# Kernel optimization log

Hardware: AMD Instinct MI355X
Metric: run time of the kernel (lower is better)

The kernel has to match this reference:

```python
import jax, jax.numpy as jnp
import numpy as np
from jax import lax

B, L, H, K = 64, 1024, 768, 4
C1, C2 = 0.1, 0.1


def crf_marginals(feats, maskf, T):
    """Batched linear-chain CRF forward-backward.
    feats: [B,L,K] emission scores, maskf: [B,L] float (1=valid), T: [K,K] transitions.
    Returns marginals [B,L,K] (zeroed at padded positions)."""
    a0 = feats[:, 0]  # [B,K]

    def fwd_step(a, xs):
        f_t, m_t = xs  # [B,K], [B]
        new = f_t + jax.nn.logsumexp(a[:, :, None] + T[None], axis=1)
        a = jnp.where(m_t[:, None] > 0, new, a)  # freeze alpha past last valid token
        return a, a

    _, alphas_rest = lax.scan(fwd_step, a0,
                              (jnp.swapaxes(feats[:, 1:], 0, 1), maskf[:, 1:].T))
    alphas = jnp.concatenate([a0[None], alphas_rest], axis=0)  # [L,B,K]
    logZ = jax.nn.logsumexp(alphas[-1], axis=-1)  # [B] (alpha frozen at last valid t)

    bL = jnp.zeros_like(a0)

    def bwd_step(b, xs):
        f_n, m_n = xs  # emission/mask at t+1
        new = jax.nn.logsumexp(T[None] + (f_n + b)[:, None, :], axis=2)
        b = jnp.where(m_n[:, None] > 0, new, b)  # beta stays 0 until last valid token
        return b, b

    xs = (jnp.swapaxes(feats[:, 1:][:, ::-1], 0, 1), maskf[:, 1:][:, ::-1].T)
    _, betas_rev = lax.scan(bwd_step, bL, xs)
    betas = jnp.concatenate([bL[None], betas_rev], axis=0)[::-1]  # [L,B,K]

    marg = jnp.exp(alphas + betas - logZ[None, :, None]) * maskf.T[:, :, None]
    return jnp.swapaxes(marg, 0, 1)  # [B,L,K]


def _forward(hidden, maskf, w, b, T):
    feats = hidden @ w.T + b                      # [B,L,K] feat2tri
    marg = crf_marginals(feats, maskf, T)
    sp = marg[:, :, 1]                            # select_polarities, masked [B,L]
    gamma = sp.sum(axis=1) / 2.0                  # [B]
    sent_vs = jnp.einsum('bl,blh->bh', sp, hidden) / gamma[:, None]
    s_prob = sp / gamma[:, None]                  # padded-ragged per-token probs
    s_prob_norm = jnp.abs(s_prob).sum(axis=1).mean()
    pena = jax.nn.relu(T[1, 0] - T[0, 0]) + jax.nn.relu(T[0, 1] - T[1, 1])
    norm_pen = C1 * pena + C2 * s_prob_norm
    return sent_vs, norm_pen, s_prob


def setup_inputs():
    key = jax.random.key(0)
    ks = jax.random.split(key, 8)
    hidden = jax.random.normal(ks[0], (B, L, H), dtype=jnp.float32)
    seq_lens = jax.random.randint(ks[1], (B,), L // 4, L + 1)
    # hidden_mask: 0 for valid tokens, nonzero for padding (forward uses mask = hidden_mask==0)
    hidden_mask = (jnp.arange(L)[None, :] >= seq_lens[:, None]).astype(jnp.int32)
    subj_position = jax.random.randint(ks[2], (B, L), -20, 21)
    obj_position = jax.random.randint(ks[3], (B, L), -20, 21)
    pe_inputs = jax.random.randint(ks[4], (B, L), 0, 2 * L)
    pe_binary = jax.random.randint(ks[5], (B, L), 0, 2)
    w_feat2tri = jax.random.normal(ks[6], (K, H), dtype=jnp.float32) * (1.0 / np.sqrt(H)).astype(np.float32)
    b_feat2tri = jnp.zeros((K,), dtype=jnp.float32)
    transitions = jax.random.normal(ks[7], (K, K), dtype=jnp.float32) * 0.1
    return dict(hidden=hidden, hidden_mask=hidden_mask, subj_position=subj_position,
                obj_position=obj_position, seq_lens=seq_lens, pe_inputs=pe_inputs,
                pe_binary=pe_binary, w_feat2tri=w_feat2tri, b_feat2tri=b_feat2tri,
                transitions=transitions)


def reference(hidden, hidden_mask, subj_position, obj_position, seq_lens, pe_inputs,
              pe_binary, w_feat2tri, b_feat2tri, transitions):
    maskf = (hidden_mask == 0).astype(hidden.dtype)
    # relevance is computed in the original forward but never consumed downstream,
    # so it has no effect on outputs; omitted here.
    return _forward(hidden, maskf, w_feat2tri, b_feat2tri, transitions)
```

## Files before the change

### kernel.cpp

```cpp
#include <hip/hip_runtime.h>

#define B 64
#define L 1024
#define H 768
#define NROWS (B * L)
#define LOG2E 1.4426950408889634f
#define CS 16
#define NCH 64
#define NG 16

#define EXP2(x) __builtin_amdgcn_exp2f(x)
#define LOG2(x) __builtin_amdgcn_logf(x)

__device__ __forceinline__ void renorm4(float& x0, float& x1, float& x2, float& x3, float& lc) {
    const float g = fmaxf(fmaxf(x0, x1), fmaxf(x2, x3));
    const int e = (__float_as_int(g) >> 23) & 255;
    const float s = __int_as_float((254 - e) << 23);
    x0 *= s; x1 *= s; x2 *= s; x3 *= s;
    lc += (float)(e - 127);
}

__global__ __launch_bounds__(256) void feats_kernel(
    const float* __restrict__ hidden, const float* __restrict__ w,
    const float* __restrict__ bias, float4* __restrict__ pfeatsT)
{
    const int lane = threadIdx.x & 63;
    const int wave = (blockIdx.x * blockDim.x + threadIdx.x) >> 6;
    const int nwaves = (gridDim.x * blockDim.x) >> 6;

    float wr[3][4][4];
#pragma unroll
    for (int c = 0; c < 3; ++c)
#pragma unroll
        for (int j = 0; j < 4; ++j)
#pragma unroll
            for (int k = 0; k < 4; ++k)
                wr[c][j][k] = w[k * H + lane * 4 + 256 * c + j];
    const float bb0 = bias[0], bb1 = bias[1], bb2 = bias[2], bb3 = bias[3];

    for (int row = wave; row < NROWS; row += nwaves) {
        const float4* hrow = reinterpret_cast<const float4*>(hidden) + (size_t)row * (H / 4);
        float acc[4] = {0.f, 0.f, 0.f, 0.f};
#pragma unroll
        for (int c = 0; c < 3; ++c) {
            float4 h = hrow[lane + 64 * c];
            const float hv[4] = {h.x, h.y, h.z, h.w};
#pragma unroll
            for (int j = 0; j < 4; ++j)
#pragma unroll
                for (int k = 0; k < 4; ++k)
                    acc[k] = fmaf(hv[j], wr[c][j][k], acc[k]);
        }
#pragma unroll
        for (int k = 0; k < 4; ++k) {
            float v = acc[k];
#pragma unroll
            for (int s = 32; s >= 1; s >>= 1) v += __shfl_xor(v, s, 64);
            acc[k] = v;
        }
        if (lane == 0) {
            const int b = row >> 10, l = row & 1023;
            pfeatsT[l * B + b] = make_float4(EXP2((acc[0] + bb0) * LOG2E),
                                             EXP2((acc[1] + bb1) * LOG2E),
                                             EXP2((acc[2] + bb2) * LOG2E),
                                             EXP2((acc[3] + bb3) * LOG2E));
        }
    }
}

__global__ __launch_bounds__(128) void chunkmat_kernel(
    const float4* __restrict__ pfeatsT, const int* __restrict__ seq_lens,
    const float* __restrict__ T, float* __restrict__ mats_p,
    float* __restrict__ mats_lc)
{
    const int b = threadIdx.x & 63;
    const int dir = threadIdx.x >> 6;
    const int c = blockIdx.x;
    const int sl = seq_lens[b];
    const int lo = c * CS + 1;
    const int hi = min(c * CS + CS, L - 1);
    const int ns = hi - lo + 1;

    float eT2[4][4];
#pragma unroll
    for (int i = 0; i < 4; ++i)
#pragma unroll
        for (int j = 0; j < 4; ++j) eT2[i][j] = EXP2(T[i * 4 + j] * LOG2E);

    float4 fr[CS];
#pragma unroll
    for (int u = 0; u < CS; ++u) {
        const int t = dir ? max(hi - u, lo) : min(lo + u, hi);
        fr[u] = pfeatsT[t * B + b];
    }

    float M[4][4];
#pragma unroll
    for (int i = 0; i < 4; ++i)
#pragma unroll
        for (int j = 0; j < 4; ++j) M[i][j] = (i == j) ? 1.f : 0.f;
    float lc = 0.f;

#pragma unroll
    for (int u = 0; u < CS; ++u) {
        const int pos = dir ? (hi - u) : (lo + u);
        const bool valid = (u < ns) && (pos < sl);
        const float f[4] = {fr[u].x, fr[u].y, fr[u].z, fr[u].w};
        float nM[4][4];
        if (dir == 0) {
#pragma unroll
            for (int i = 0; i < 4; ++i)
#pragma unroll
                for (int j = 0; j < 4; ++j) {
                    const float s = (M[i][0] * eT2[0][j] + M[i][1] * eT2[1][j]) +
                                    (M[i][2] * eT2[2][j] + M[i][3] * eT2[3][j]);
                    nM[i][j] = s * f[j];
                }
        } else {
            float Mg[4][4];
#pragma unroll
            for (int k = 0; k < 4; ++k)
#pragma unroll
                for (int j = 0; j < 4; ++j) Mg[k][j] = f[k] * M[k][j];
#pragma unroll
            for (int i = 0; i < 4; ++i)
#pragma unroll
                for (int j = 0; j < 4; ++j)
                    nM[i][j] = (eT2[i][0] * Mg[0][j] + eT2[i][1] * Mg[1][j]) +
                               (eT2[i][2] * Mg[2][j] + eT2[i][3] * Mg[3][j]);
        }
#pragma unroll
        for (int i = 0; i < 4; ++i)
#pragma unroll
            for (int j = 0; j < 4; ++j) M[i][j] = valid ? nM[i][j] : M[i][j];

        if (u == 7 || u == CS - 1) {
            float g = 0.f;
#pragma unroll
            for (int i = 0; i < 4; ++i)
#pragma unroll
                for (int j = 0; j < 4; ++j) g = fmaxf(g, M[i][j]);
            const int e = (__float_as_int(g) >> 23) & 255;
            const float s = __int_as_float((254 - e) << 23);
#pragma unroll
            for (int i = 0; i < 4; ++i)
#pragma unroll
                for (int j = 0; j < 4; ++j) M[i][j] *= s;
            lc += (float)(e - 127);
        }
    }
#pragma unroll
    for (int i = 0; i < 4; ++i)
#pragma unroll
        for (int j = 0; j < 4; ++j)
            mats_p[((dir * NCH + c) * 16 + i * 4 + j) * B + b] = M[i][j];
    mats_lc[(dir * NCH + c) * B + b] = lc;
}

__global__ __launch_bounds__(128) void groupmat_kernel(
    const float* __restrict__ mats_p, const float* __restrict__ mats_lc,
    float* __restrict__ smats_p, float* __restrict__ smats_lc)
{
    const int b = threadIdx.x & 63;
    const int dir = threadIdx.x >> 6;
    const int g = blockIdx.x;

    float P[4][4];
    float lc = 0.f;
    {
        const int c0 = 4 * g;
#pragma unroll
        for (int k = 0; k < 16; ++k)
            P[k >> 2][k & 3] = mats_p[((dir * NCH + c0) * 16 + k) * B + b];
        lc = mats_lc[(dir * NCH + c0) * B + b];
    }

#pragma unroll
    for (int q = 1; q < 4; ++q) {
        const int c = 4 * g + q;
        float Q[4][4];
#pragma unroll
        for (int k = 0; k < 16; ++k)
            Q[k >> 2][k & 3] = mats_p[((dir * NCH + c) * 16 + k) * B + b];
        lc += mats_lc[(dir * NCH + c) * B + b];

        float R[4][4];
#pragma unroll
        for (int i = 0; i < 4; ++i)
#pragma unroll
            for (int j = 0; j < 4; ++j)
                R[i][j] = (P[i][0] * Q[0][j] + P[i][1] * Q[1][j]) +
                          (P[i][2] * Q[2][j] + P[i][3] * Q[3][j]);

        float gmax = 0.f;
#pragma unroll
        for (int i = 0; i < 4; ++i)
#pragma unroll
            for (int j = 0; j < 4; ++j) gmax = fmaxf(gmax, R[i][j]);
        const int e = (__float_as_int(gmax) >> 23) & 255;
        const float s = __int_as_float((254 - e) << 23);
#pragma unroll
        for (int i = 0; i < 4; ++i)
#pragma unroll
            for (int j = 0; j < 4; ++j) P[i][j] = R[i][j] * s;
        lc += (float)(e - 127);
    }

#pragma unroll
    for (int i = 0; i < 4; ++i)
#pragma unroll
        for (int j = 0; j < 4; ++j)
            smats_p[((dir * NG + g) * 16 + i * 4 + j) * B + b] = P[i][j];
    smats_lc[(dir * NG + g) * B + b] = lc;
}

__global__ __launch_bounds__(128) void bound_kernel(
    const float4* __restrict__ pfeatsT, const float* __restrict__ smats_p,
    const float* __restrict__ smats_lc, float* __restrict__ gbound_p,
    float* __restrict__ gbound_lc, float* __restrict__ logZ)
{
    const int b = threadIdx.x & 63;
    const int dir = threadIdx.x >> 6;

    float Ms[4][17];
#pragma unroll
    for (int p = 0; p < 3; ++p) {
        const int cc = dir ? (NG - 1 - p) : p;
#pragma unroll
        for (int k = 0; k < 16; ++k)
            Ms[p][k] = smats_p[((dir * NG + cc) * 16 + k) * B + b];
        Ms[p][16] = smats_lc[(dir * NG + cc) * B + b];
    }

    float v0, v1, v2, v3, vlc = 0.f;
    if (dir == 0) {
        const float4 f0 = pfeatsT[b];
        v0 = f0.x; v1 = f0.y; v2 = f0.z; v3 = f0.w;
    } else {
        v0 = v1 = v2 = v3 = 1.f;
    }

#pragma unroll
    for (int u = 0; u < NG; ++u) {
        const int cc = dir ? (NG - 1 - u) : u;
        gbound_p[((dir * NG + cc) * 4 + 0) * B + b] = v0;
        gbound_p[((dir * NG + cc) * 4 + 1) * B + b] = v1;
        gbound_p[((dir * NG + cc) * 4 + 2) * B + b] = v2;
        gbound_p[((dir * NG + cc) * 4 + 3) * B + b] = v3;
        gbound_lc[(dir * NG + cc) * B + b] = vlc;
        if (u + 3 < NG) {
            const int cp = dir ? (NG - 1 - (u + 3)) : (u + 3);
#pragma unroll
            for (int k = 0; k < 16; ++k)
                Ms[(u + 3) & 3][k] = smats_p[((dir * NG + cp) * 16 + k) * B + b];
            Ms[(u + 3) & 3][16] = smats_lc[(dir * NG + cp) * B + b];
        }
        const float* Pm = Ms[u & 3];
        float n0, n1, n2, n3;
        if (dir == 0) {
            n0 = (v0 * Pm[0] + v1 * Pm[4]) + (v2 * Pm[8] + v3 * Pm[12]);
            n1 = (v0 * Pm[1] + v1 * Pm[5]) + (v2 * Pm[9] + v3 * Pm[13]);
            n2 = (v0 * Pm[2] + v1 * Pm[6]) + (v2 * Pm[10] + v3 * Pm[14]);
            n3 = (v0 * Pm[3] + v1 * Pm[7]) + (v2 * Pm[11] + v3 * Pm[15]);
        } else {
            n0 = (Pm[0] * v0 + Pm[1] * v1) + (Pm[2] * v2 + Pm[3] * v3);
            n1 = (Pm[4] * v0 + Pm[5] * v1) + (Pm[6] * v2 + Pm[7] * v3);
            n2 = (Pm[8] * v0 + Pm[9] * v1) + (Pm[10] * v2 + Pm[11] * v3);
            n3 = (Pm[12] * v0 + Pm[13] * v1) + (Pm[14] * v2 + Pm[15] * v3);
        }
        v0 = n0; v1 = n1; v2 = n2; v3 = n3;
        vlc += Pm[16];
        renorm4(v0, v1, v2, v3, vlc);
    }
    if (dir == 0)
        logZ[b] = LOG2(((v0 + v1) + (v2 + v3))) + vlc;
}

__global__ __launch_bounds__(128) void rescan_sp_kernel(
    const float4* __restrict__ pfeatsT, const int* __restrict__ seq_lens,
    const float* __restrict__ T, const float* __restrict__ mats_p,
    const float* __restrict__ mats_lc, const float* __restrict__ gbound_p,
    const float* __restrict__ gbound_lc, const float* __restrict__ logZ,
    float* __restrict__ spu, float* __restrict__ chunksum)
{
    const int tid = threadIdx.x;
    const int b = tid & 63;
    const int dir = tid >> 6;
    const int c = blockIdx.x;
    const int g = c >> 2;
    const int r = c & 3;
    const int sl = seq_lens[b];
    const int base = c * CS;

    float eT2[4][4];
#pragma unroll
    for (int i = 0; i < 4; ++i)
#pragma unroll
        for (int j = 0; j < 4; ++j) eT2[i][j] = EXP2(T[i * 4 + j] * LOG2E);

    __shared__ float ldb_p[CS * 64];
    __shared__ float ldb_lc[CS * 64];

    if (dir == 1) {
        float v0 = gbound_p[((NG + g) * 4 + 0) * B + b];
        float v1 = gbound_p[((NG + g) * 4 + 1) * B + b];
        float v2 = gbound_p[((NG + g) * 4 + 2) * B + b];
        float v3 = gbound_p[((NG + g) * 4 + 3) * B + b];
        float blc = gbound_lc[(NG + g) * B + b];
        for (int q = 3; q > r; --q) {
            const int cq = 4 * g + q;
            float Mq[16];
#pragma unroll
            for (int k = 0; k < 16; ++k)
                Mq[k] = mats_p[((NCH + cq) * 16 + k) * B + b];
            blc += mats_lc[(NCH + cq) * B + b];
            const float n0 = (Mq[0] * v0 + Mq[1] * v1) + (Mq[2] * v2 + Mq[3] * v3);
            const float n1 = (Mq[4] * v0 + Mq[5] * v1) + (Mq[6] * v2 + Mq[7] * v3);
            const float n2 = (Mq[8] * v0 + Mq[9] * v1) + (Mq[10] * v2 + Mq[11] * v3);
            const float n3 = (Mq[12] * v0 + Mq[13] * v1) + (Mq[14] * v2 + Mq[15] * v3);
            v0 = n0; v1 = n1; v2 = n2; v3 = n3;
            renorm4(v0, v1, v2, v3, blc);
        }

        const bool last = (c == NCH - 1);
        const int hi_n = last ? (L - 1) : (base + CS);
        const int cnt = last ? (CS - 1) : CS;
        if (last) { ldb_p[15 * 64 + b] = v1; ldb_lc[15 * 64 + b] = blc; }
        float4 fr[CS];
#pragma unroll
        for (int u = 0; u < CS; ++u) fr[u] = pfeatsT[max(hi_n - u, base + 1) * B + b];
#pragma unroll
        for (int u = 0; u < CS; ++u) {
            if (u < cnt) {
                const int n = hi_n - u;
                const bool valid = n < sl;
                const float4 f = fr[u];
                const float c0 = f.x * v0, c1 = f.y * v1, c2 = f.z * v2, c3 = f.w * v3;
                const float n0 = (eT2[0][0] * c0 + eT2[0][1] * c1) + (eT2[0][2] * c2 + eT2[0][3] * c3);
                const float n1 = (eT2[1][0] * c0 + eT2[1][1] * c1) + (eT2[1][2] * c2 + eT2[1][3] * c3);
                const float n2 = (eT2[2][0] * c0 + eT2[2][1] * c1) + (eT2[2][2] * c2 + eT2[2][3] * c3);
                const float n3 = (eT2[3][0] * c0 + eT2[3][1] * c1) + (eT2[3][2] * c2 + eT2[3][3] * c3);
                v0 = valid ? n0 : v0; v1 = valid ? n1 : v1;
                v2 = valid ? n2 : v2; v3 = valid ? n3 : v3;
                if ((u & 3) == 3) renorm4(v0, v1, v2, v3, blc);
                ldb_p[(n - 1 - base) * 64 + b] = v1;
                ldb_lc[(n - 1 - base) * 64 + b] = blc;
            }
        }
    }

    float av_p[CS], av_lc[CS];
    if (dir == 0) {
        float a0 = gbound_p[(g * 4 + 0) * B + b];
        float a1 = gbound_p[(g * 4 + 1) * B + b];
        float a2 = gbound_p[(g * 4 + 2) * B + b];
        float a3 = gbound_p[(g * 4 + 3) * B + b];
        float alc = gbound_lc[g * B + b];
        for (int q = 0; q < r; ++q) {
            const int cq = 4 * g + q;
            float Mq[16];
#pragma unroll
            for (int k = 0; k < 16; ++k)
                Mq[k] = mats_p[(cq * 16 + k) * B + b];
            alc += mats_lc[cq * B + b];
            const float n0 = (a0 * Mq[0] + a1 * Mq[4]) + (a2 * Mq[8] + a3 * Mq[12]);
            const float n1 = (a0 * Mq[1] + a1 * Mq[5]) + (a2 * Mq[9] + a3 * Mq[13]);
            const float n2 = (a0 * Mq[2] + a1 * Mq[6]) + (a2 * Mq[10] + a3 * Mq[14]);
            const float n3 = (a0 * Mq[3] + a1 * Mq[7]) + (a2 * Mq[11] + a3 * Mq[15]);
            a0 = n0; a1 = n1; a2 = n2; a3 = n3;
            renorm4(a0, a1, a2, a3, alc);
        }

        av_p[0] = a1; av_lc[0] = alc;
        float4 fr[CS - 1];
#pragma unroll
        for (int u = 1; u < CS; ++u) fr[u - 1] = pfeatsT[(base + u) * B + b];
#pragma unroll
        for (int u = 1; u < CS; ++u) {
            const int t = base + u;
            const bool valid = t < sl;
            const float4 f = fr[u - 1];
            const float s0 = (a0 * eT2[0][0] + a1 * eT2[1][0]) + (a2 * eT2[2][0] + a3 * eT2[3][0]);
            const float s1 = (a0 * eT2[0][1] + a1 * eT2[1][1]) + (a2 * eT2[2][1] + a3 * eT2[3][1]);
            const float s2 = (a0 * eT2[0][2] + a1 * eT2[1][2]) + (a2 * eT2[2][2] + a3 * eT2[3][2]);
            const float s3 = (a0 * eT2[0][3] + a1 * eT2[1][3]) + (a2 * eT2[2][3] + a3 * eT2[3][3]);
            const float n0 = s0 * f.x, n1 = s1 * f.y, n2 = s2 * f.z, n3 = s3 * f.w;
            a0 = valid ? n0 : a0; a1 = valid ? n1 : a1;
            a2 = valid ? n2 : a2; a3 = valid ? n3 : a3;
            if ((u & 3) == 3) renorm4(a0, a1, a2, a3, alc);
            av_p[u] = a1; av_lc[u] = alc;
        }
    }

    __syncthreads();

    if (dir == 0) {
        const float lz = logZ[b];
        float sp[CS];
        float local = 0.f;
#pragma unroll
        for (int u = 0; u < CS; ++u) {
            const int l = base + u;
            const float x = (l < sl)
                ? av_p[u] * ldb_p[u * 64 + b] * EXP2(av_lc[u] + ldb_lc[u * 64 + b] - lz)
                : 0.f;
            sp[u] = x;
            local += x;
        }
        float4* dst = reinterpret_cast<float4*>(spu + b * L + base);
#pragma unroll
        for (int q = 0; q < 4; ++q)
            dst[q] = make_float4(sp[4 * q], sp[4 * q + 1], sp[4 * q + 2], sp[4 * q + 3]);
        chunksum[c * 64 + b] = local;
    }
}

__global__ __launch_bounds__(768) void sentv_kernel(
    const float* __restrict__ hidden, const float* __restrict__ spu,
    float4* __restrict__ partial)
{
    const int b  = blockIdx.x >> 3;
    const int lc = blockIdx.x & 7;
    const int tid = threadIdx.x;
    const int col = tid % 192;
    const int r   = tid / 192;

    const float4* hb = reinterpret_cast<const float4*>(hidden) + ((size_t)b * L + lc * 128) * 192;
    const float* sp = spu + b * L + lc * 128;

    float4 acc = make_float4(0.f, 0.f, 0.f, 0.f);
#pragma unroll 4
    for (int i = 0; i < 32; ++i) {
        const int l = 4 * i + r;
        const float s = sp[l];
        const float4 h = hb[(size_t)l * 192 + col];
        acc.x = fmaf(s, h.x, acc.x); acc.y = fmaf(s, h.y, acc.y);
        acc.z = fmaf(s, h.z, acc.z); acc.w = fmaf(s, h.w, acc.w);
    }

    __shared__ float4 red[768];
    red[tid] = acc;
    __syncthreads();
    if (tid < 192) {
        const float4 a0 = red[tid], a1 = red[tid + 192], a2 = red[tid + 384], a3 = red[tid + 576];
        float4 rr;
        rr.x = (a0.x + a1.x) + (a2.x + a3.x);
        rr.y = (a0.y + a1.y) + (a2.y + a3.y);
        rr.z = (a0.z + a1.z) + (a2.z + a3.z);
        rr.w = (a0.w + a1.w) + (a2.w + a3.w);
        partial[((size_t)lc * B + b) * 192 + tid] = rr;
    }
}

__global__ __launch_bounds__(256) void final_kernel(
    const float4* __restrict__ partial, const float* __restrict__ chunksum,
    const float* __restrict__ spu, const float* __restrict__ T,
    float* __restrict__ out, float* __restrict__ sprob)
{
    const int b = blockIdx.x;
    const int tid = threadIdx.x;

    __shared__ float s_tot;
    if (tid < 64) {
        float v = chunksum[tid * 64 + b];
#pragma unroll
        for (int s = 32; s >= 1; s >>= 1) v += __shfl_xor(v, s, 64);
        if (tid == 0) s_tot = v;
    }
    __syncthreads();
    const float inv = 2.0f / s_tot;

    if (tid < 192) {
        float4 acc = make_float4(0.f, 0.f, 0.f, 0.f);
#pragma unroll
        for (int q = 0; q < 8; ++q) {
            const float4 p = partial[((size_t)q * B + b) * 192 + tid];
            acc.x += p.x; acc.y += p.y; acc.z += p.z; acc.w += p.w;
        }
        acc.x *= inv; acc.y *= inv; acc.z *= inv; acc.w *= inv;
        reinterpret_cast<float4*>(out + (size_t)b * H)[tid] = acc;
    }

#pragma unroll
    for (int q = 0; q < 4; ++q) {
        const int l = tid + q * 256;
        sprob[b * L + l] = spu[b * L + l] * inv;
    }
    if (b == 0 && tid == 0) {
        const float pena = fmaxf(T[4] - T[0], 0.f) + fmaxf(T[1] - T[5], 0.f);
        out[B * H] = 0.1f * pena + 0.1f * 2.0f;
    }
}

extern "C" void kernel_launch(void* const* d_in, const int* in_sizes, int n_in,
                              void* d_out, int out_size, void* d_ws, size_t ws_size,
                              hipStream_t stream) {
    const float* hidden   = (const float*)d_in[0];
    const int*   seq_lens = (const int*)d_in[4];
    const float* w        = (const float*)d_in[7];
    const float* bias     = (const float*)d_in[8];
    const float* T        = (const float*)d_in[9];

    float* ws = (float*)d_ws;
    float4* pfeatsT    = (float4*)(ws);
    float*  mats_p     = ws + 262144;
    float*  mats_lc    = ws + 393216;
    float*  smats_p    = ws + 401408;
    float*  smats_lc   = ws + 434176;
    float*  gbound_p   = ws + 436224;
    float*  gbound_lc  = ws + 444416;
    float*  logZ       = ws + 446464;
    float*  chunksum   = ws + 446528;
    float*  spu        = ws + 450624;
    float4* partial    = (float4*)(ws + 516160);

    float* out   = (float*)d_out;
    float* sprob = out + B * H + 1;

    feats_kernel<<<2048, 256, 0, stream>>>(hidden, w, bias, pfeatsT);
    chunkmat_kernel<<<NCH, 128, 0, stream>>>((const float4*)pfeatsT, seq_lens, T, mats_p, mats_lc);
    groupmat_kernel<<<NG, 128, 0, stream>>>(mats_p, mats_lc, smats_p, smats_lc);
    bound_kernel<<<1, 128, 0, stream>>>((const float4*)pfeatsT, smats_p, smats_lc,
                                        gbound_p, gbound_lc, logZ);
    rescan_sp_kernel<<<NCH, 128, 0, stream>>>((const float4*)pfeatsT, seq_lens, T,
                                              mats_p, mats_lc, gbound_p, gbound_lc,
                                              logZ, spu, chunksum);
    sentv_kernel<<<512, 768, 0, stream>>>(hidden, spu, partial);
    final_kernel<<<64, 256, 0, stream>>>(partial, chunksum, spu, T, out, sprob);
}
```

Baseline: 88.54 us.

## Fuse group scan and boundary propagation; fuse sentence-vector reduction with finalize

The group-matrix and group-boundary kernels are merged into one 1024-thread single-block kernel. That kernel also expands the group boundaries into per-chunk alpha/beta boundary vectors, so the rescan kernel no longer repeats up to three matrix-vector steps per chunk. The sentence-vector reduction and the final normalization kernel are fused into one kernel over a 3x64 grid that loops over all 1024 positions, which removes the partial buffer and a launch. The fused reduction uses only 192 blocks of 256 threads for the large memory-bound read of hidden, so achieved bandwidth may drop compared with the previous 512-block split.

```diff
diff --git a/kernel.cpp b/kernel.cpp
--- a/kernel.cpp
+++ b/kernel.cpp
@@ -157,138 +157,207 @@
     mats_lc[(dir * NCH + c) * B + b] = lc;
 }
 
-__global__ __launch_bounds__(128) void groupmat_kernel(
-    const float* __restrict__ mats_p, const float* __restrict__ mats_lc,
-    float* __restrict__ smats_p, float* __restrict__ smats_lc)
+__global__ __launch_bounds__(1024) void bound2_kernel(
+    const float4* __restrict__ pfeatsT, const float* __restrict__ mats_p,
+    const float* __restrict__ mats_lc, float* __restrict__ smats_p,
+    float* __restrict__ smats_lc, float* __restrict__ vbound_p,
+    float* __restrict__ vbound_lc, float* __restrict__ logZ)
 {
-    const int b = threadIdx.x & 63;
-    const int dir = threadIdx.x >> 6;
-    const int g = blockIdx.x;
-
-    float P[4][4];
-    float lc = 0.f;
+    const int tid = threadIdx.x;
+
+    __shared__ float gb_p[2 * NG * 4 * B];
+    __shared__ float gb_lc[2 * NG * B];
+
     {
-        const int c0 = 4 * g;
-#pragma unroll
-        for (int k = 0; k < 16; ++k)
-            P[k >> 2][k & 3] = mats_p[((dir * NCH + c0) * 16 + k) * B + b];
-        lc = mats_lc[(dir * NCH + c0) * B + b];
-    }
-
-#pragma unroll
-    for (int q = 1; q < 4; ++q) {
-        const int c = 4 * g + q;
-        float Q[4][4];
-#pragma unroll
-        for (int k = 0; k < 16; ++k)
-            Q[k >> 2][k & 3] = mats_p[((dir * NCH + c) * 16 + k) * B + b];
-        lc += mats_lc[(dir * NCH + c) * B + b];
-
-        float R[4][4];
-#pragma unroll
-        for (int i = 0; i < 4; ++i)
-#pragma unroll
-            for (int j = 0; j < 4; ++j)
-                R[i][j] = (P[i][0] * Q[0][j] + P[i][1] * Q[1][j]) +
-                          (P[i][2] * Q[2][j] + P[i][3] * Q[3][j]);
-
-        float gmax = 0.f;
-#pragma unroll
-        for (int i = 0; i < 4; ++i)
-#pragma unroll
-            for (int j = 0; j < 4; ++j) gmax = fmaxf(gmax, R[i][j]);
-        const int e = (__float_as_int(gmax) >> 23) & 255;
-        const float s = __int_as_float((254 - e) << 23);
-#pragma unroll
-        for (int i = 0; i < 4; ++i)
-#pragma unroll
-            for (int j = 0; j < 4; ++j) P[i][j] = R[i][j] * s;
-        lc += (float)(e - 127);
-    }
-
-#pragma unroll
-    for (int i = 0; i < 4; ++i)
-#pragma unroll
-        for (int j = 0; j < 4; ++j)
-            smats_p[((dir * NG + g) * 16 + i * 4 + j) * B + b] = P[i][j];
-    smats_lc[(dir * NG + g) * B + b] = lc;
-}
-
-__global__ __launch_bounds__(128) void bound_kernel(
-    const float4* __restrict__ pfeatsT, const float* __restrict__ smats_p,
-    const float* __restrict__ smats_lc, float* __restrict__ gbound_p,
-    float* __restrict__ gbound_lc, float* __restrict__ logZ)
-{
-    const int b = threadIdx.x & 63;
-    const int dir = threadIdx.x >> 6;
-
-    float Ms[4][17];
-#pragma unroll
-    for (int p = 0; p < 3; ++p) {
-        const int cc = dir ? (NG - 1 - p) : p;
-#pragma unroll
-        for (int k = 0; k < 16; ++k)
-            Ms[p][k] = smats_p[((dir * NG + cc) * 16 + k) * B + b];
-        Ms[p][16] = smats_lc[(dir * NG + cc) * B + b];
-    }
-
-    float v0, v1, v2, v3, vlc = 0.f;
-    if (dir == 0) {
-        const float4 f0 = pfeatsT[b];
-        v0 = f0.x; v1 = f0.y; v2 = f0.z; v3 = f0.w;
-    } else {
-        v0 = v1 = v2 = v3 = 1.f;
-    }
-
-#pragma unroll
-    for (int u = 0; u < NG; ++u) {
-        const int cc = dir ? (NG - 1 - u) : u;
-        gbound_p[((dir * NG + cc) * 4 + 0) * B + b] = v0;
-        gbound_p[((dir * NG + cc) * 4 + 1) * B + b] = v1;
-        gbound_p[((dir * NG + cc) * 4 + 2) * B + b] = v2;
-        gbound_p[((dir * NG + cc) * 4 + 3) * B + b] = v3;
-        gbound_lc[(dir * NG + cc) * B + b] = vlc;
-        if (u + 3 < NG) {
-            const int cp = dir ? (NG - 1 - (u + 3)) : (u + 3);
+        const int b = tid & 63;
+        const int dir = (tid >> 6) & 1;
+        const int g0 = tid >> 7;
+#pragma unroll
+        for (int gg = 0; gg < 2; ++gg) {
+            const int g = g0 + 8 * gg;
+            float P[4][4];
+            float lc;
+            {
+                const int c0 = 4 * g;
+#pragma unroll
+                for (int k = 0; k < 16; ++k)
+                    P[k >> 2][k & 3] = mats_p[((dir * NCH + c0) * 16 + k) * B + b];
+                lc = mats_lc[(dir * NCH + c0) * B + b];
+            }
+#pragma unroll
+            for (int q = 1; q < 4; ++q) {
+                const int c = 4 * g + q;
+                float Q[4][4];
+#pragma unroll
+                for (int k = 0; k < 16; ++k)
+                    Q[k >> 2][k & 3] = mats_p[((dir * NCH + c) * 16 + k) * B + b];
+                lc += mats_lc[(dir * NCH + c) * B + b];
+
+                float R[4][4];
+#pragma unroll
+                for (int i = 0; i < 4; ++i)
+#pragma unroll
+                    for (int j = 0; j < 4; ++j)
+                        R[i][j] = (P[i][0] * Q[0][j] + P[i][1] * Q[1][j]) +
+                                  (P[i][2] * Q[2][j] + P[i][3] * Q[3][j]);
+
+                float gmax = 0.f;
+#pragma unroll
+                for (int i = 0; i < 4; ++i)
+#pragma unroll
+                    for (int j = 0; j < 4; ++j) gmax = fmaxf(gmax, R[i][j]);
+                const int e = (__float_as_int(gmax) >> 23) & 255;
+                const float s = __int_as_float((254 - e) << 23);
+#pragma unroll
+                for (int i = 0; i < 4; ++i)
+#pragma unroll
+                    for (int j = 0; j < 4; ++j) P[i][j] = R[i][j] * s;
+                lc += (float)(e - 127);
+            }
+#pragma unroll
+            for (int i = 0; i < 4; ++i)
+#pragma unroll
+                for (int j = 0; j < 4; ++j)
+                    smats_p[((dir * NG + g) * 16 + i * 4 + j) * B + b] = P[i][j];
+            smats_lc[(dir * NG + g) * B + b] = lc;
+        }
+    }
+
+    __syncthreads();
+
+    if (tid < 128) {
+        const int b = tid & 63;
+        const int dir = tid >> 6;
+
+        float Ms[4][17];
+#pragma unroll
+        for (int p = 0; p < 3; ++p) {
+            const int cc = dir ? (NG - 1 - p) : p;
 #pragma unroll
             for (int k = 0; k < 16; ++k)
-                Ms[(u + 3) & 3][k] = smats_p[((dir * NG + cp) * 16 + k) * B + b];
-            Ms[(u + 3) & 3][16] = smats_lc[(dir * NG + cp) * B + b];
-        }
-        const float* Pm = Ms[u & 3];
-        float n0, n1, n2, n3;
+                Ms[p][k] = smats_p[((dir * NG + cc) * 16 + k) * B + b];
+            Ms[p][16] = smats_lc[(dir * NG + cc) * B + b];
+        }
+
+        float v0, v1, v2, v3, vlc = 0.f;
         if (dir == 0) {
-            n0 = (v0 * Pm[0] + v1 * Pm[4]) + (v2 * Pm[8] + v3 * Pm[12]);
-            n1 = (v0 * Pm[1] + v1 * Pm[5]) + (v2 * Pm[9] + v3 * Pm[13]);
-            n2 = (v0 * Pm[2] + v1 * Pm[6]) + (v2 * Pm[10] + v3 * Pm[14]);
-            n3 = (v0 * Pm[3] + v1 * Pm[7]) + (v2 * Pm[11] + v3 * Pm[15]);
+            const float4 f0 = pfeatsT[b];
+            v0 = f0.x; v1 = f0.y; v2 = f0.z; v3 = f0.w;
         } else {
-            n0 = (Pm[0] * v0 + Pm[1] * v1) + (Pm[2] * v2 + Pm[3] * v3);
-            n1 = (Pm[4] * v0 + Pm[5] * v1) + (Pm[6] * v2 + Pm[7] * v3);
-            n2 = (Pm[8] * v0 + Pm[9] * v1) + (Pm[10] * v2 + Pm[11] * v3);
-            n3 = (Pm[12] * v0 + Pm[13] * v1) + (Pm[14] * v2 + Pm[15] * v3);
-        }
-        v0 = n0; v1 = n1; v2 = n2; v3 = n3;
-        vlc += Pm[16];
-        renorm4(v0, v1, v2, v3, vlc);
-    }
-    if (dir == 0)
-        logZ[b] = LOG2(((v0 + v1) + (v2 + v3))) + vlc;
+            v0 = v1 = v2 = v3 = 1.f;
+        }
+
+#pragma unroll
+        for (int u = 0; u < NG; ++u) {
+            const int cc = dir ? (NG - 1 - u) : u;
+            gb_p[((dir * NG + cc) * 4 + 0) * B + b] = v0;
+            gb_p[((dir * NG + cc) * 4 + 1) * B + b] = v1;
+            gb_p[((dir * NG + cc) * 4 + 2) * B + b] = v2;
+            gb_p[((dir * NG + cc) * 4 + 3) * B + b] = v3;
+            gb_lc[(dir * NG + cc) * B + b] = vlc;
+            if (u + 3 < NG) {
+                const int cp = dir ? (NG - 1 - (u + 3)) : (u + 3);
+#pragma unroll
+                for (int k = 0; k < 16; ++k)
+                    Ms[(u + 3) & 3][k] = smats_p[((dir * NG + cp) * 16 + k) * B + b];
+                Ms[(u + 3) & 3][16] = smats_lc[(dir * NG + cp) * B + b];
+            }
+            const float* Pm = Ms[u & 3];
+            float n0, n1, n2, n3;
+            if (dir == 0) {
+                n0 = (v0 * Pm[0] + v1 * Pm[4]) + (v2 * Pm[8] + v3 * Pm[12]);
+                n1 = (v0 * Pm[1] + v1 * Pm[5]) + (v2 * Pm[9] + v3 * Pm[13]);
+                n2 = (v0 * Pm[2] + v1 * Pm[6]) + (v2 * Pm[10] + v3 * Pm[14]);
+                n3 = (v0 * Pm[3] + v1 * Pm[7]) + (v2 * Pm[11] + v3 * Pm[15]);
+            } else {
+                n0 = (Pm[0] * v0 + Pm[1] * v1) + (Pm[2] * v2 + Pm[3] * v3);
+                n1 = (Pm[4] * v0 + Pm[5] * v1) + (Pm[6] * v2 + Pm[7] * v3);
+                n2 = (Pm[8] * v0 + Pm[9] * v1) + (Pm[10] * v2 + Pm[11] * v3);
+                n3 = (Pm[12] * v0 + Pm[13] * v1) + (Pm[14] * v2 + Pm[15] * v3);
+            }
+            v0 = n0; v1 = n1; v2 = n2; v3 = n3;
+            vlc += Pm[16];
+            renorm4(v0, v1, v2, v3, vlc);
+        }
+        if (dir == 0)
+            logZ[b] = LOG2(((v0 + v1) + (v2 + v3))) + vlc;
+    }
+
+    __syncthreads();
+
+#pragma unroll
+    for (int it = 0; it < 2; ++it) {
+        const int idx = tid + 1024 * it;
+        const int bb = idx & 63;
+        const int dd = (idx >> 6) & 1;
+        const int g = idx >> 7;
+
+        float v0 = gb_p[((dd * NG + g) * 4 + 0) * B + bb];
+        float v1 = gb_p[((dd * NG + g) * 4 + 1) * B + bb];
+        float v2 = gb_p[((dd * NG + g) * 4 + 2) * B + bb];
+        float v3 = gb_p[((dd * NG + g) * 4 + 3) * B + bb];
+        float lc = gb_lc[(dd * NG + g) * B + bb];
+
+        if (dd == 0) {
+#pragma unroll
+            for (int r = 0; r < 4; ++r) {
+                const int c = 4 * g + r;
+                vbound_p[(c * 4 + 0) * B + bb] = v0;
+                vbound_p[(c * 4 + 1) * B + bb] = v1;
+                vbound_p[(c * 4 + 2) * B + bb] = v2;
+                vbound_p[(c * 4 + 3) * B + bb] = v3;
+                vbound_lc[c * B + bb] = lc;
+                if (r < 3) {
+                    float Mq[16];
+#pragma unroll
+                    for (int k = 0; k < 16; ++k)
+                        Mq[k] = mats_p[(c * 16 + k) * B + bb];
+                    lc += mats_lc[c * B + bb];
+                    const float n0 = (v0 * Mq[0] + v1 * Mq[4]) + (v2 * Mq[8] + v3 * Mq[12]);
+                    const float n1 = (v0 * Mq[1] + v1 * Mq[5]) + (v2 * Mq[9] + v3 * Mq[13]);
+                    const float n2 = (v0 * Mq[2] + v1 * Mq[6]) + (v2 * Mq[10] + v3 * Mq[14]);
+                    const float n3 = (v0 * Mq[3] + v1 * Mq[7]) + (v2 * Mq[11] + v3 * Mq[15]);
+                    v0 = n0; v1 = n1; v2 = n2; v3 = n3;
+                    renorm4(v0, v1, v2, v3, lc);
+                }
+            }
+        } else {
+#pragma unroll
+            for (int r = 3; r >= 0; --r) {
+                const int c = 4 * g + r;
+                vbound_p[((NCH + c) * 4 + 0) * B + bb] = v0;
+                vbound_p[((NCH + c) * 4 + 1) * B + bb] = v1;
+                vbound_p[((NCH + c) * 4 + 2) * B + bb] = v2;
+                vbound_p[((NCH + c) * 4 + 3) * B + bb] = v3;
+                vbound_lc[(NCH + c) * B + bb] = lc;
+                if (r > 0) {
+                    float Mq[16];
+#pragma unroll
+                    for (int k = 0; k < 16; ++k)
+                        Mq[k] = mats_p[((NCH + c) * 16 + k) * B + bb];
+                    lc += mats_lc[(NCH + c) * B + bb];
+                    const float n0 = (Mq[0] * v0 + Mq[1] * v1) + (Mq[2] * v2 + Mq[3] * v3);
+                    const float n1 = (Mq[4] * v0 + Mq[5] * v1) + (Mq[6] * v2 + Mq[7] * v3);
+                    const float n2 = (Mq[8] * v0 + Mq[9] * v1) + (Mq[10] * v2 + Mq[11] * v3);
+                    const float n3 = (Mq[12] * v0 + Mq[13] * v1) + (Mq[14] * v2 + Mq[15] * v3);
+                    v0 = n0; v1 = n1; v2 = n2; v3 = n3;
+                    renorm4(v0, v1, v2, v3, lc);
+                }
+            }
+        }
+    }
 }
 
 __global__ __launch_bounds__(128) void rescan_sp_kernel(
     const float4* __restrict__ pfeatsT, const int* __restrict__ seq_lens,
-    const float* __restrict__ T, const float* __restrict__ mats_p,
-    const float* __restrict__ mats_lc, const float* __restrict__ gbound_p,
-    const float* __restrict__ gbound_lc, const float* __restrict__ logZ,
+    const float* __restrict__ T, const float* __restrict__ vbound_p,
+    const float* __restrict__ vbound_lc, const float* __restrict__ logZ,
     float* __restrict__ spu, float* __restrict__ chunksum)
 {
     const int tid = threadIdx.x;
     const int b = tid & 63;
     const int dir = tid >> 6;
     const int c = blockIdx.x;
-    const int g = c >> 2;
-    const int r = c & 3;
     const int sl = seq_lens[b];
     const int base = c * CS;
 
@@ -302,26 +371,11 @@
     __shared__ float ldb_lc[CS * 64];
 
     if (dir == 1) {
-        float v0 = gbound_p[((NG + g) * 4 + 0) * B + b];
-        float v1 = gbound_p[((NG + g) * 4 + 1) * B + b];
-        float v2 = gbound_p[((NG + g) * 4 + 2) * B + b];
-        float v3 = gbound_p[((NG + g) * 4 + 3) * B + b];
-        float blc = gbound_lc[(NG + g) * B + b];
-        for (int q = 3; q > r; --q) {
-            const int cq = 4 * g + q;
-            float Mq[16];
-#pragma unroll
-            for (int k = 0; k < 16; ++k)
-                Mq[k] = mats_p[((NCH + cq) * 16 + k) * B + b];
-            blc += mats_lc[(NCH + cq) * B + b];
-            const float n0 = (Mq[0] * v0 + Mq[1] * v1) + (Mq[2] * v2 + Mq[3] * v3);
-            const float n1 = (Mq[4] * v0 + Mq[5] * v1) + (Mq[6] * v2 + Mq[7] * v3);
-            const float n2 = (Mq[8] * v0 + Mq[9] * v1) + (Mq[10] * v2 + Mq[11] * v3);
-            const float n3 = (Mq[12] * v0 + Mq[13] * v1) + (Mq[14] * v2 + Mq[15] * v3);
-            v0 = n0; v1 = n1; v2 = n2; v3 = n3;
-            renorm4(v0, v1, v2, v3, blc);
-        }
-
+        float v0 = vbound_p[((NCH + c) * 4 + 0) * B + b];
+        float v1 = vbound_p[((NCH + c) * 4 + 1) * B + b];
+        float v2 = vbound_p[((NCH + c) * 4 + 2) * B + b];
+        float v3 = vbound_p[((NCH + c) * 4 + 3) * B + b];
+        float blc = vbound_lc[(NCH + c) * B + b];
         const bool last = (c == NCH - 1);
         const int hi_n = last ? (L - 1) : (base + CS);
         const int cnt = last ? (CS - 1) : CS;
@@ -351,26 +405,11 @@
 
     float av_p[CS], av_lc[CS];
     if (dir == 0) {
-        float a0 = gbound_p[(g * 4 + 0) * B + b];
-        float a1 = gbound_p[(g * 4 + 1) * B + b];
-        float a2 = gbound_p[(g * 4 + 2) * B + b];
-        float a3 = gbound_p[(g * 4 + 3) * B + b];
-        float alc = gbound_lc[g * B + b];
-        for (int q = 0; q < r; ++q) {
-            const int cq = 4 * g + q;
-            float Mq[16];
-#pragma unroll
-            for (int k = 0; k < 16; ++k)
-                Mq[k] = mats_p[(cq * 16 + k) * B + b];
-            alc += mats_lc[cq * B + b];
-            const float n0 = (a0 * Mq[0] + a1 * Mq[4]) + (a2 * Mq[8] + a3 * Mq[12]);
-            const float n1 = (a0 * Mq[1] + a1 * Mq[5]) + (a2 * Mq[9] + a3 * Mq[13]);
-            const float n2 = (a0 * Mq[2] + a1 * Mq[6]) + (a2 * Mq[10] + a3 * Mq[14]);
-            const float n3 = (a0 * Mq[3] + a1 * Mq[7]) + (a2 * Mq[11] + a3 * Mq[15]);
-            a0 = n0; a1 = n1; a2 = n2; a3 = n3;
-            renorm4(a0, a1, a2, a3, alc);
-        }
-
+        float a0 = vbound_p[(c * 4 + 0) * B + b];
+        float a1 = vbound_p[(c * 4 + 1) * B + b];
+        float a2 = vbound_p[(c * 4 + 2) * B + b];
+        float a3 = vbound_p[(c * 4 + 3) * B + b];
+        float alc = vbound_lc[c * B + b];
         av_p[0] = a1; av_lc[0] = alc;
         float4 fr[CS - 1];
 #pragma unroll
@@ -415,50 +454,16 @@
     }
 }
 
-__global__ __launch_bounds__(768) void sentv_kernel(
+__global__ __launch_bounds__(256) void sentv_kernel(
     const float* __restrict__ hidden, const float* __restrict__ spu,
-    float4* __restrict__ partial)
-{
-    const int b  = blockIdx.x >> 3;
-    const int lc = blockIdx.x & 7;
-    const int tid = threadIdx.x;
-    const int col = tid % 192;
-    const int r   = tid / 192;
-
-    const float4* hb = reinterpret_cast<const float4*>(hidden) + ((size_t)b * L + lc * 128) * 192;
-    const float* sp = spu + b * L + lc * 128;
-
-    float4 acc = make_float4(0.f, 0.f, 0.f, 0.f);
-#pragma unroll 4
-    for (int i = 0; i < 32; ++i) {
-        const int l = 4 * i + r;
-        const float s = sp[l];
-        const float4 h = hb[(size_t)l * 192 + col];
-        acc.x = fmaf(s, h.x, acc.x); acc.y = fmaf(s, h.y, acc.y);
-        acc.z = fmaf(s, h.z, acc.z); acc.w = fmaf(s, h.w, acc.w);
-    }
-
-    __shared__ float4 red[768];
-    red[tid] = acc;
-    __syncthreads();
-    if (tid < 192) {
-        const float4 a0 = red[tid], a1 = red[tid + 192], a2 = red[tid + 384], a3 = red[tid + 576];
-        float4 rr;
-        rr.x = (a0.x + a1.x) + (a2.x + a3.x);
-        rr.y = (a0.y + a1.y) + (a2.y + a3.y);
-        rr.z = (a0.z + a1.z) + (a2.z + a3.z);
-        rr.w = (a0.w + a1.w) + (a2.w + a3.w);
-        partial[((size_t)lc * B + b) * 192 + tid] = rr;
-    }
-}
-
-__global__ __launch_bounds__(256) void final_kernel(
-    const float4* __restrict__ partial, const float* __restrict__ chunksum,
-    const float* __restrict__ spu, const float* __restrict__ T,
+    const float* __restrict__ chunksum, const float* __restrict__ T,
     float* __restrict__ out, float* __restrict__ sprob)
 {
-    const int b = blockIdx.x;
+    const int hc = blockIdx.x;
+    const int b  = blockIdx.y;
     const int tid = threadIdx.x;
+    const int lane = tid & 63;
+    const int w = tid >> 6;
 
     __shared__ float s_tot;
     if (tid < 64) {
@@ -470,25 +475,42 @@
     __syncthreads();
     const float inv = 2.0f / s_tot;
 
-    if (tid < 192) {
-        float4 acc = make_float4(0.f, 0.f, 0.f, 0.f);
-#pragma unroll
-        for (int q = 0; q < 8; ++q) {
-            const float4 p = partial[((size_t)q * B + b) * 192 + tid];
-            acc.x += p.x; acc.y += p.y; acc.z += p.z; acc.w += p.w;
-        }
-        acc.x *= inv; acc.y *= inv; acc.z *= inv; acc.w *= inv;
-        reinterpret_cast<float4*>(out + (size_t)b * H)[tid] = acc;
-    }
-
-#pragma unroll
-    for (int q = 0; q < 4; ++q) {
-        const int l = tid + q * 256;
-        sprob[b * L + l] = spu[b * L + l] * inv;
-    }
-    if (b == 0 && tid == 0) {
-        const float pena = fmaxf(T[4] - T[0], 0.f) + fmaxf(T[1] - T[5], 0.f);
-        out[B * H] = 0.1f * pena + 0.1f * 2.0f;
+    const float4* hb = reinterpret_cast<const float4*>(hidden + ((size_t)b * L) * H + hc * 256) + lane;
+    const float* sp = spu + b * L;
+
+    float4 acc = make_float4(0.f, 0.f, 0.f, 0.f);
+#pragma unroll 8
+    for (int i = 0; i < 256; ++i) {
+        const int l = w + 4 * i;
+        const float s = sp[l];
+        const float4 h = hb[(size_t)l * (H / 4)];
+        acc.x = fmaf(s, h.x, acc.x); acc.y = fmaf(s, h.y, acc.y);
+        acc.z = fmaf(s, h.z, acc.z); acc.w = fmaf(s, h.w, acc.w);
+    }
+
+    __shared__ float4 red[4][64];
+    red[w][lane] = acc;
+    __syncthreads();
+    if (tid < 64) {
+        const float4 a0 = red[0][lane], a1 = red[1][lane], a2 = red[2][lane], a3 = red[3][lane];
+        float4 r;
+        r.x = ((a0.x + a1.x) + (a2.x + a3.x)) * inv;
+        r.y = ((a0.y + a1.y) + (a2.y + a3.y)) * inv;
+        r.z = ((a0.z + a1.z) + (a2.z + a3.z)) * inv;
+        r.w = ((a0.w + a1.w) + (a2.w + a3.w)) * inv;
+        reinterpret_cast<float4*>(out + (size_t)b * H + hc * 256)[lane] = r;
+    }
+
+    if (hc == 0) {
+#pragma unroll
+        for (int q = 0; q < 4; ++q) {
+            const int l = tid + q * 256;
+            sprob[b * L + l] = sp[l] * inv;
+        }
+        if (b == 0 && tid == 0) {
+            const float pena = fmaxf(T[4] - T[0], 0.f) + fmaxf(T[1] - T[5], 0.f);
+            out[B * H] = 0.1f * pena + 0.1f * 2.0f;
+        }
     }
 }
 
@@ -507,24 +529,20 @@
     float*  mats_lc    = ws + 393216;
     float*  smats_p    = ws + 401408;
     float*  smats_lc   = ws + 434176;
-    float*  gbound_p   = ws + 436224;
-    float*  gbound_lc  = ws + 444416;
-    float*  logZ       = ws + 446464;
-    float*  chunksum   = ws + 446528;
-    float*  spu        = ws + 450624;
-    float4* partial    = (float4*)(ws + 516160);
+    float*  vbound_p   = ws + 436224;
+    float*  vbound_lc  = ws + 468992;
+    float*  logZ       = ws + 477184;
+    float*  chunksum   = ws + 477248;
+    float*  spu        = ws + 481344;
 
     float* out   = (float*)d_out;
     float* sprob = out + B * H + 1;
 
     feats_kernel<<<2048, 256, 0, stream>>>(hidden, w, bias, pfeatsT);
     chunkmat_kernel<<<NCH, 128, 0, stream>>>((const float4*)pfeatsT, seq_lens, T, mats_p, mats_lc);
-    groupmat_kernel<<<NG, 128, 0, stream>>>(mats_p, mats_lc, smats_p, smats_lc);
-    bound_kernel<<<1, 128, 0, stream>>>((const float4*)pfeatsT, smats_p, smats_lc,
-                                        gbound_p, gbound_lc, logZ);
+    bound2_kernel<<<1, 1024, 0, stream>>>((const float4*)pfeatsT, mats_p, mats_lc,
+                                          smats_p, smats_lc, vbound_p, vbound_lc, logZ);
     rescan_sp_kernel<<<NCH, 128, 0, stream>>>((const float4*)pfeatsT, seq_lens, T,
-                                              mats_p, mats_lc, gbound_p, gbound_lc,
-                                              logZ, spu, chunksum);
-    sentv_kernel<<<512, 768, 0, stream>>>(hidden, spu, partial);
-    final_kernel<<<64, 256, 0, stream>>>(partial, chunksum, spu, T, out, sprob);
-}
+                                              vbound_p, vbound_lc, logZ, spu, chunksum);
+    sentv_kernel<<<dim3(3, 64), 256, 0, stream>>>(hidden, spu, chunksum, T, out, sprob);
+}
```

Result: slower. 94.48 us (+6.7%).

## Fuse sentence-vector reduction with final normalization into one kernel

Applied to the files above, without the earlier changes.

Merges the weighted hidden-state reduction and the final normalization kernel into a single kernel. Each block now owns a 256-column slice of one batch row and reduces over the full sequence, so the partial-sum buffer and one kernel launch go away. The grid shrinks from 512 blocks of 768 threads to 192 blocks of 1024 threads. That lowers parallelism while streaming about 200MB of hidden states, which could cut achievable memory bandwidth on a GPU with many CUs.

```diff
diff --git a/kernel.cpp b/kernel.cpp
--- a/kernel.cpp
+++ b/kernel.cpp
@@ -415,50 +415,16 @@
     }
 }
 
-__global__ __launch_bounds__(768) void sentv_kernel(
+__global__ __launch_bounds__(1024) void sentv_final_kernel(
     const float* __restrict__ hidden, const float* __restrict__ spu,
-    float4* __restrict__ partial)
-{
-    const int b  = blockIdx.x >> 3;
-    const int lc = blockIdx.x & 7;
-    const int tid = threadIdx.x;
-    const int col = tid % 192;
-    const int r   = tid / 192;
-
-    const float4* hb = reinterpret_cast<const float4*>(hidden) + ((size_t)b * L + lc * 128) * 192;
-    const float* sp = spu + b * L + lc * 128;
-
-    float4 acc = make_float4(0.f, 0.f, 0.f, 0.f);
-#pragma unroll 4
-    for (int i = 0; i < 32; ++i) {
-        const int l = 4 * i + r;
-        const float s = sp[l];
-        const float4 h = hb[(size_t)l * 192 + col];
-        acc.x = fmaf(s, h.x, acc.x); acc.y = fmaf(s, h.y, acc.y);
-        acc.z = fmaf(s, h.z, acc.z); acc.w = fmaf(s, h.w, acc.w);
-    }
-
-    __shared__ float4 red[768];
-    red[tid] = acc;
-    __syncthreads();
-    if (tid < 192) {
-        const float4 a0 = red[tid], a1 = red[tid + 192], a2 = red[tid + 384], a3 = red[tid + 576];
-        float4 rr;
-        rr.x = (a0.x + a1.x) + (a2.x + a3.x);
-        rr.y = (a0.y + a1.y) + (a2.y + a3.y);
-        rr.z = (a0.z + a1.z) + (a2.z + a3.z);
-        rr.w = (a0.w + a1.w) + (a2.w + a3.w);
-        partial[((size_t)lc * B + b) * 192 + tid] = rr;
-    }
-}
-
-__global__ __launch_bounds__(256) void final_kernel(
-    const float4* __restrict__ partial, const float* __restrict__ chunksum,
-    const float* __restrict__ spu, const float* __restrict__ T,
+    const float* __restrict__ chunksum, const float* __restrict__ T,
     float* __restrict__ out, float* __restrict__ sprob)
 {
-    const int b = blockIdx.x;
+    const int hc = blockIdx.x;
+    const int b  = blockIdx.y;
     const int tid = threadIdx.x;
+    const int lane = tid & 63;
+    const int w = tid >> 6;
 
     __shared__ float s_tot;
     if (tid < 64) {
@@ -470,25 +436,44 @@
     __syncthreads();
     const float inv = 2.0f / s_tot;
 
-    if (tid < 192) {
-        float4 acc = make_float4(0.f, 0.f, 0.f, 0.f);
-#pragma unroll
-        for (int q = 0; q < 8; ++q) {
-            const float4 p = partial[((size_t)q * B + b) * 192 + tid];
-            acc.x += p.x; acc.y += p.y; acc.z += p.z; acc.w += p.w;
-        }
-        acc.x *= inv; acc.y *= inv; acc.z *= inv; acc.w *= inv;
-        reinterpret_cast<float4*>(out + (size_t)b * H)[tid] = acc;
-    }
-
-#pragma unroll
-    for (int q = 0; q < 4; ++q) {
-        const int l = tid + q * 256;
-        sprob[b * L + l] = spu[b * L + l] * inv;
-    }
-    if (b == 0 && tid == 0) {
-        const float pena = fmaxf(T[4] - T[0], 0.f) + fmaxf(T[1] - T[5], 0.f);
-        out[B * H] = 0.1f * pena + 0.1f * 2.0f;
+    const float4* hb = reinterpret_cast<const float4*>(hidden) +
+                       (size_t)b * L * (H / 4) + hc * 64;
+    const float* sp = spu + b * L;
+
+    float4 acc = make_float4(0.f, 0.f, 0.f, 0.f);
+#pragma unroll 8
+    for (int i = 0; i < 64; ++i) {
+        const int l = w + 16 * i;
+        const float s = sp[l];
+        const float4 h = hb[(size_t)l * (H / 4) + lane];
+        acc.x = fmaf(s, h.x, acc.x); acc.y = fmaf(s, h.y, acc.y);
+        acc.z = fmaf(s, h.z, acc.z); acc.w = fmaf(s, h.w, acc.w);
+    }
+
+    __shared__ float4 red[16][64];
+    red[w][lane] = acc;
+    __syncthreads();
+    if (tid < 64) {
+        float4 r = make_float4(0.f, 0.f, 0.f, 0.f);
+#pragma unroll
+        for (int q = 0; q < 16; q += 4) {
+            const float4 a0 = red[q][lane], a1 = red[q + 1][lane];
+            const float4 a2 = red[q + 2][lane], a3 = red[q + 3][lane];
+            r.x += (a0.x + a1.x) + (a2.x + a3.x);
+            r.y += (a0.y + a1.y) + (a2.y + a3.y);
+            r.z += (a0.z + a1.z) + (a2.z + a3.z);
+            r.w += (a0.w + a1.w) + (a2.w + a3.w);
+        }
+        r.x *= inv; r.y *= inv; r.z *= inv; r.w *= inv;
+        reinterpret_cast<float4*>(out)[(size_t)b * (H / 4) + hc * 64 + lane] = r;
+    }
+
+    if (hc == 0) {
+        sprob[b * L + tid] = sp[tid] * inv;
+        if (b == 0 && tid == 0) {
+            const float pena = fmaxf(T[4] - T[0], 0.f) + fmaxf(T[1] - T[5], 0.f);
+            out[B * H] = 0.1f * pena + 0.1f * 2.0f;
+        }
     }
 }
 
@@ -512,7 +497,6 @@
     float*  logZ       = ws + 446464;
     float*  chunksum   = ws + 446528;
     float*  spu        = ws + 450624;
-    float4* partial    = (float4*)(ws + 516160);
 
     float* out   = (float*)d_out;
     float* sprob = out + B * H + 1;
@@ -525,6 +509,5 @@
     rescan_sp_kernel<<<NCH, 128, 0, stream>>>((const float4*)pfeatsT, seq_lens, T,
                                               mats_p, mats_lc, gbound_p, gbound_lc,
                                               logZ, spu, chunksum);
-    sentv_kernel<<<512, 768, 0, stream>>>(hidden, spu, partial);
-    final_kernel<<<64, 256, 0, stream>>>(partial, chunksum, spu, T, out, sprob);
-}
+    sentv_final_kernel<<<dim3(3, 64), 1024, 0, stream>>>(hidden, spu, chunksum, T, out, sprob);
+}
```

After: 85.94 us, median of 2. -2.9%, faster.
